# Performance work log

Measured on AMD Instinct MI355X. Metric: run time of the kernel, lower is better.

## Reference

```python
import jax, jax.numpy as jnp
import numpy as np

NUM_SCALES = 7
WEIGHTS = [1.0] * 7


def get_m(r, c):
    # r, c: [B, H, W] float coords; density map is [B, a, a], a = min(H, W)
    B, H, W = r.shape
    a = min(H, W)
    N = H * W
    xf = jnp.clip(jnp.floor(r), 0, a - 1).astype(jnp.int32)
    yf = jnp.clip(jnp.floor(c), 0, a - 1).astype(jnp.int32)
    xc = jnp.clip(jnp.ceil(r), 0, a - 1).astype(jnp.int32)
    yc = jnp.clip(jnp.ceil(c), 0, a - 1).astype(jnp.int32)
    xw = r - xf.astype(r.dtype)
    yw = c - yf.astype(c.dtype)
    w_tl = (1 - xw) * (1 - yw)
    w_tr = xw * (1 - yw)
    w_bl = (1 - xw) * yw
    w_br = xw * yw
    idx = jnp.concatenate([
        (xf * a + yf).reshape(B, N), (xc * a + yf).reshape(B, N),
        (xf * a + yc).reshape(B, N), (xc * a + yc).reshape(B, N)], axis=1)
    w = jnp.concatenate([
        w_tl.reshape(B, N), w_tr.reshape(B, N),
        w_bl.reshape(B, N), w_br.reshape(B, N)], axis=1)
    dm = jnp.zeros((B, a * a), dtype=r.dtype)
    dm = dm.at[jnp.arange(B)[:, None], idx].add(w)
    return dm.reshape(B, a, a)


def masked_bce(pred, tgt):
    # torch F.binary_cross_entropy clamps log terms at -100
    p = pred.reshape(-1)
    t = tgt.reshape(-1)
    log_p = jnp.clip(jnp.log(p), -100.0, None)
    log_1mp = jnp.clip(jnp.log(1.0 - p), -100.0, None)
    bce = -(t * log_p + (1.0 - t) * log_1mp)
    valid = (t == 1.0).astype(p.dtype)
    return jnp.sum(bce * valid) / jnp.sum(valid)


def _multiscale_loss(r3, c3, r4, c4, target):
    B = target.shape[0]
    Ht, Wt = target.shape[2], target.shape[3]
    total = 0.0
    for i in range(NUM_SCALES):
        cm = get_m(r3[i], c3[i]) + get_m(r4[i], c4[i])
        cm = cm / cm.max()
        resized = jax.image.resize(cm[:, None, :, :], (B, 1, Ht, Wt), method='linear')
        total = total + WEIGHTS[i] * masked_bce(resized, target)
    return total


def setup_inputs() -> dict:
    key = jax.random.key(0)
    k1, k2, k3, k4, k5 = jax.random.split(key, 5)
    a = 512
    shp = (NUM_SCALES, 8, a, a)
    scale = float(a - 1)
    r3 = jax.random.uniform(k1, shp, dtype=jnp.float32) * scale
    c3 = jax.random.uniform(k2, shp, dtype=jnp.float32) * scale
    r4 = jax.random.uniform(k3, shp, dtype=jnp.float32) * scale
    c4 = jax.random.uniform(k4, shp, dtype=jnp.float32) * scale
    target = (jax.random.uniform(k5, (8, 1, a, a)) < 0.5).astype(jnp.float32)
    return {"r3": r3, "c3": c3, "r4": r4, "c4": c4, "target": target}


def reference(r3, c3, r4, c4, target):
    return _multiscale_loss(r3, c3, r4, c4, target)
```

## Files before the change

kernel.cpp:

```cpp
#include <hip/hip_runtime.h>
#include <math.h>

#define A      512
#define NB     8
#define NS     7
#define AA     (A*A)
#define PPS    (NB*AA)
#define RPS    15
#define NSTRIP 35
#define LROWS  16
#define NIMG   (NS*NB)
#define NBKT   (NIMG*NSTRIP)
#define CAP    16896
#define BIN_THR 256
#define PTS_PER_BLOCK 4096
#define SPLAT_THR 512
#define SCALE_F   33554432.0f
#define INV_SCALE (1.0f/33554432.0f)
#define MAXB   1024
#define BCEB   2048

#define PARTS_OFF_F  2048
#define PARTS2_OFF_F 12288
#define NVAL_OFF_F   12800
#define BCEP_OFF_F   16384
#define DM_OFF_F     32768
#define BKT_OFF    ((size_t)DM_OFF_F * 4 + (size_t)NS * PPS * 4)
#define PER_IMG_B  ((size_t)NSTRIP * CAP * 8)

__global__ void init_kernel(float* __restrict__ ws) {
    if (blockIdx.x == 0) {
        for (int i = threadIdx.x; i < 2048; i += 128) ws[i] = 0.f;
        return;
    }
    int bkt = blockIdx.x - 1;
    int img = bkt / NSTRIP, k = bkt % NSTRIP;
    float4* row = (float4*)(ws + DM_OFF_F + (size_t)img * AA + (k * RPS) * A);
    row[threadIdx.x] = make_float4(0, 0, 0, 0);
}

__global__ void __launch_bounds__(BIN_THR)
bin_kernel(const float4* __restrict__ r3, const float4* __restrict__ c3,
           const float4* __restrict__ r4, const float4* __restrict__ c4,
           unsigned* __restrict__ cursors, float2* __restrict__ buckets,
           int img0) {
    const int limg = blockIdx.y;
    const int img  = img0 + limg;
    const float4* rp = blockIdx.z ? r4 : r3;
    const float4* cp = blockIdx.z ? c4 : c3;
    const int qbase = img * (AA / 4) + blockIdx.x * (PTS_PER_BLOCK / 4);

    float4 r[4], c[4];
#pragma unroll
    for (int j = 0; j < 4; j++) {
        int q = qbase + j * BIN_THR + threadIdx.x;
        r[j] = rp[q]; c[j] = cp[q];
    }

    __shared__ unsigned lcur[NSTRIP], lbase[NSTRIP];
    if (threadIdx.x < NSTRIP) lcur[threadIdx.x] = 0;
    __syncthreads();

    unsigned slot[16];
#define ALLOC(idx, rv) slot[idx] = atomicAdd(&lcur[(int)(rv) / RPS], 1u)
#pragma unroll
    for (int j = 0; j < 4; j++) {
        ALLOC(j * 4 + 0, r[j].x); ALLOC(j * 4 + 1, r[j].y);
        ALLOC(j * 4 + 2, r[j].z); ALLOC(j * 4 + 3, r[j].w);
    }
#undef ALLOC
    __syncthreads();

    if (threadIdx.x < NSTRIP)
        lbase[threadIdx.x] =
            atomicAdd(&cursors[img * NSTRIP + threadIdx.x], lcur[threadIdx.x]);
    __syncthreads();

    const int lbkt0 = limg * NSTRIP;
#define EMIT(idx, rv, cv) {                                                   \
        int s = (int)(rv) / RPS;                                              \
        unsigned sl = lbase[s] + slot[idx];                                   \
        if (sl < CAP)                                                         \
            buckets[(size_t)(lbkt0 + s) * CAP + sl] = make_float2(rv, cv); }
#pragma unroll
    for (int j = 0; j < 4; j++) {
        EMIT(j * 4 + 0, r[j].x, c[j].x); EMIT(j * 4 + 1, r[j].y, c[j].y);
        EMIT(j * 4 + 2, r[j].z, c[j].z); EMIT(j * 4 + 3, r[j].w, c[j].w);
    }
#undef EMIT
}

__device__ __forceinline__ void splat_pt(unsigned long long cp[2][LROWS][A/2],
                                         int g0, float r, float c) {
    int xf = (int)r, yf = (int)c;
    float xw = r - (float)xf, yw = c - (float)yf;
    float omx = 1.f - xw, omy = 1.f - yw;
    unsigned q0 = (unsigned)(omx * omy * SCALE_F + 0.5f);
    unsigned q1 = (unsigned)(omx * yw  * SCALE_F + 0.5f);
    unsigned q2 = (unsigned)(xw  * omy * SCALE_F + 0.5f);
    unsigned q3 = (unsigned)(xw  * yw  * SCALE_F + 0.5f);
    int lr = xf - g0, sel = yf & 1, pp = yf >> 1;
    atomicAdd(&cp[sel][lr    ][pp], ((unsigned long long)q1 << 32) | q0);
    atomicAdd(&cp[sel][lr + 1][pp], ((unsigned long long)q3 << 32) | q2);
}

__device__ __forceinline__ void combine4(unsigned long long cp[2][LROWS][A/2],
                                         int j, int c4, float v[4]) {
#pragma unroll
    for (int t = 0; t < 4; t++) {
        int cc = c4 + t;
        unsigned long long e = cp[0][j][cc >> 1];
        unsigned s = (cc & 1) ? (unsigned)(e >> 32) : (unsigned)e;
        if (cc & 1) s += (unsigned)cp[1][j][cc >> 1];
        else if (cc >= 2) s += (unsigned)(cp[1][j][(cc >> 1) - 1] >> 32);
        v[t] = (float)s * INV_SCALE;
    }
}

__global__ void __launch_bounds__(SPLAT_THR)
splat_dense(const float2* __restrict__ buckets, const unsigned* __restrict__ cursors,
            float* __restrict__ dm, const float4* __restrict__ tgt,
            float4* __restrict__ parts, int img0) {
    __shared__ unsigned long long cp[2][LROWS][A / 2];
    __shared__ float sr[8][3];
    const int lbkt = blockIdx.x;
    const int limg = lbkt / NSTRIP, k = lbkt % NSTRIP;
    const int img  = img0 + limg;
    const int b    = img & 7;
    const int g0   = k * RPS;

    unsigned long long* z = &cp[0][0][0];
    for (int i = threadIdx.x; i < 2 * LROWS * (A / 2); i += SPLAT_THR) z[i] = 0ull;
    __syncthreads();

    unsigned n = cursors[img * NSTRIP + k]; if (n > CAP) n = CAP;
    const float4* bp4 = (const float4*)(buckets + (size_t)lbkt * CAP);
    unsigned n2 = (n + 1) >> 1;
    for (unsigned i = threadIdx.x; i < n2; i += SPLAT_THR) {
        float4 q = bp4[i];
        splat_pt(cp, g0, q.x, q.y);
        if (2 * i + 1 < n) splat_pt(cp, g0, q.z, q.w);
    }
    __syncthreads();

    float* dimg = dm + (size_t)img * AA;
    for (int u = threadIdx.x; u < 2 * (A / 4); u += SPLAT_THR) {
        int j = (u >= (A / 4)) ? RPS : 0;
        int c4 = (u & (A / 4 - 1)) << 2;
        int gr = g0 + j;
        if (gr >= A) continue;
        float v[4];
        combine4(cp, j, c4, v);
        float* dst = dimg + gr * A + c4;
        unsafeAtomicAdd(dst + 0, v[0]); unsafeAtomicAdd(dst + 1, v[1]);
        unsafeAtomicAdd(dst + 2, v[2]); unsafeAtomicAdd(dst + 3, v[3]);
    }

    float S = 0.f, Np = 0.f, mxv = 0.f;
    const float4* timg = tgt + (size_t)b * (AA / 4);
    for (int u = threadIdx.x; u < (RPS - 1) * (A / 4); u += SPLAT_THR) {
        int j = 1 + (u >> 7), cq = u & 127, gr = g0 + j;
        if (gr >= A) continue;
        float v[4];
        combine4(cp, j, cq << 2, v);
        mxv = fmaxf(mxv, fmaxf(fmaxf(v[0], v[1]), fmaxf(v[2], v[3])));
        float4 t = timg[gr * (A / 4) + cq];
        if (t.x == 1.f && v[0] > 0.f) { S += __logf(v[0]); Np += 1.f; }
        if (t.y == 1.f && v[1] > 0.f) { S += __logf(v[1]); Np += 1.f; }
        if (t.z == 1.f && v[2] > 0.f) { S += __logf(v[2]); Np += 1.f; }
        if (t.w == 1.f && v[3] > 0.f) { S += __logf(v[3]); Np += 1.f; }
    }
    for (int off = 32; off > 0; off >>= 1) {
        S += __shfl_down(S, off); Np += __shfl_down(Np, off);
        mxv = fmaxf(mxv, __shfl_down(mxv, off));
    }
    int lane = threadIdx.x & 63, w = threadIdx.x >> 6;
    if (lane == 0) { sr[w][0] = S; sr[w][1] = Np; sr[w][2] = mxv; }
    __syncthreads();
    if (threadIdx.x == 0) {
        for (int ww = 1; ww < 8; ww++) {
            S += sr[ww][0]; Np += sr[ww][1]; mxv = fmaxf(mxv, sr[ww][2]);
        }
        parts[img * NSTRIP + k] = make_float4(S, Np, mxv, 0.f);
    }
}

__global__ void __launch_bounds__(256)
cleanup_kernel(const float* __restrict__ dm, const float4* __restrict__ tgt,
               float4* __restrict__ parts2, float* __restrict__ nval) {
    const int bx = blockIdx.x;
    float a0 = 0.f, a1 = 0.f, a2 = 0.f;
    if (bx < NIMG) {
        const int img = bx, b = img & 7;
        const float4* dimg = (const float4*)(dm + (size_t)img * AA);
        const float4* timg = tgt + (size_t)b * (AA / 4);
        for (int u = threadIdx.x; u < NSTRIP * (A / 4); u += 256) {
            int kk = u >> 7, cq = u & 127, gr = kk * RPS;
            float4 d = dimg[gr * (A / 4) + cq];
            float4 t = timg[gr * (A / 4) + cq];
            a2 = fmaxf(a2, fmaxf(fmaxf(d.x, d.y), fmaxf(d.z, d.w)));
            if (t.x == 1.f && d.x > 0.f) { a0 += __logf(d.x); a1 += 1.f; }
            if (t.y == 1.f && d.y > 0.f) { a0 += __logf(d.y); a1 += 1.f; }
            if (t.z == 1.f && d.z > 0.f) { a0 += __logf(d.z); a1 += 1.f; }
            if (t.w == 1.f && d.w > 0.f) { a0 += __logf(d.w); a1 += 1.f; }
        }
    } else {
        const float4* timg = tgt + (size_t)(bx - NIMG) * (AA / 4);
        for (int u = threadIdx.x; u < AA / 4; u += 256) {
            float4 t = timg[u];
            a0 += ((t.x == 1.f) ? 1.f : 0.f) + ((t.y == 1.f) ? 1.f : 0.f) +
                  ((t.z == 1.f) ? 1.f : 0.f) + ((t.w == 1.f) ? 1.f : 0.f);
        }
    }
    for (int off = 32; off > 0; off >>= 1) {
        a0 += __shfl_down(a0, off); a1 += __shfl_down(a1, off);
        a2 = fmaxf(a2, __shfl_down(a2, off));
    }
    __shared__ float sr[4][3];
    int lane = threadIdx.x & 63, w = threadIdx.x >> 6;
    if (lane == 0) { sr[w][0] = a0; sr[w][1] = a1; sr[w][2] = a2; }
    __syncthreads();
    if (threadIdx.x == 0) {
        for (int ww = 1; ww < 4; ww++) {
            a0 += sr[ww][0]; a1 += sr[ww][1]; a2 = fmaxf(a2, sr[ww][2]);
        }
        if (bx < NIMG) parts2[bx] = make_float4(a0, a1, a2, 0.f);
        else           nval[bx - NIMG] = a0;
    }
}

__global__ void __launch_bounds__(256)
final_fused(const float4* __restrict__ parts, const float4* __restrict__ parts2,
            const float* __restrict__ nval, float* __restrict__ out) {
    __shared__ float red[4][3];
    __shared__ float ps[NS][3];
    const int lane = threadIdx.x & 63, w = threadIdx.x >> 6;
    for (int s = 0; s < NS; s++) {
        float S = 0.f, Np = 0.f, Mx = 0.f;
        for (int t = threadIdx.x; t < NB * NSTRIP; t += 256) {
            float4 p = parts[s * NB * NSTRIP + t];
            S += p.x; Np += p.y; Mx = fmaxf(Mx, p.z);
        }
        if (threadIdx.x < NB) {
            float4 p = parts2[s * NB + threadIdx.x];
            S += p.x; Np += p.y; Mx = fmaxf(Mx, p.z);
        }
        for (int off = 32; off > 0; off >>= 1) {
            S += __shfl_down(S, off); Np += __shfl_down(Np, off);
            Mx = fmaxf(Mx, __shfl_down(Mx, off));
        }
        if (lane == 0) { red[w][0] = S; red[w][1] = Np; red[w][2] = Mx; }
        __syncthreads();
        if (threadIdx.x == 0) {
            for (int ww = 1; ww < 4; ww++) {
                S += red[ww][0]; Np += red[ww][1]; Mx = fmaxf(Mx, red[ww][2]);
            }
            ps[s][0] = S; ps[s][1] = Np; ps[s][2] = Mx;
        }
        __syncthreads();
    }
    if (threadIdx.x == 0) {
        float Nv = 0.f;
        for (int b = 0; b < NB; b++) Nv += nval[b];
        float t = 0.f;
        for (int s = 0; s < NS; s++) {
            float lm = __logf(ps[s][2]);
            t += (ps[s][1] * lm - ps[s][0] + 100.f * (Nv - ps[s][1])) / Nv;
        }
        out[0] = t;
    }
}

__device__ __forceinline__ void splat_lds_f(float lds[LROWS][A], int g0, unsigned k,
                                            float r, float c) {
    int xf = (int)r;
    if ((unsigned)xf / RPS != k) return;
    int yf = (int)c;
    float xw = r - (float)xf, yw = c - (float)yf;
    float omx = 1.f - xw, omy = 1.f - yw;
    int lr = xf - g0;
    atomicAdd(&lds[lr    ][yf    ], omx * omy);
    atomicAdd(&lds[lr + 1][yf    ], xw  * omy);
    atomicAdd(&lds[lr    ][yf + 1], omx * yw);
    atomicAdd(&lds[lr + 1][yf + 1], xw  * yw);
}

__global__ void __launch_bounds__(SPLAT_THR)
splat_gather(const float4* __restrict__ r3, const float4* __restrict__ c3,
             const float4* __restrict__ r4, const float4* __restrict__ c4,
             float* __restrict__ dm) {
    __shared__ float lds[LROWS][A];
    const unsigned k = blockIdx.x;
    const int img = blockIdx.y, tid = threadIdx.x, g0 = (int)k * RPS;
    float4* l4 = (float4*)&lds[0][0];
    for (int i = tid; i < LROWS * A / 4; i += SPLAT_THR) l4[i] = make_float4(0, 0, 0, 0);
    __syncthreads();
    const int qbase = img * (AA / 4);
    for (int i = tid; i < AA / 4; i += SPLAT_THR) {
        float4 ra = r3[qbase + i], ca = c3[qbase + i];
        float4 rb = r4[qbase + i], cb = c4[qbase + i];
        splat_lds_f(lds, g0, k, ra.x, ca.x); splat_lds_f(lds, g0, k, ra.y, ca.y);
        splat_lds_f(lds, g0, k, ra.z, ca.z); splat_lds_f(lds, g0, k, ra.w, ca.w);
        splat_lds_f(lds, g0, k, rb.x, cb.x); splat_lds_f(lds, g0, k, rb.y, cb.y);
        splat_lds_f(lds, g0, k, rb.z, cb.z); splat_lds_f(lds, g0, k, rb.w, cb.w);
    }
    __syncthreads();
    float* dimg = dm + (size_t)img * AA;
    for (int u = tid; u < LROWS * (A / 4); u += SPLAT_THR) {
        int j = u >> 7, cq = u & 127, gr = g0 + j;
        if (gr >= A) continue;
        float4 v = ((float4*)&lds[j][0])[cq];
        float* dst = dimg + gr * A + cq * 4;
        if (j == 0 || j == RPS) {
            unsafeAtomicAdd(dst + 0, v.x); unsafeAtomicAdd(dst + 1, v.y);
            unsafeAtomicAdd(dst + 2, v.z); unsafeAtomicAdd(dst + 3, v.w);
        } else {
            *(float4*)dst = v;
        }
    }
}

__global__ void max_kernel(const float4* __restrict__ dm, float* __restrict__ maxp) {
    int s = blockIdx.y;
    const float4* p = dm + (size_t)s * (PPS / 4);
    float m = 0.f;
    for (int i = blockIdx.x * blockDim.x + threadIdx.x; i < PPS / 4;
         i += gridDim.x * blockDim.x) {
        float4 v = p[i];
        m = fmaxf(m, fmaxf(fmaxf(v.x, v.y), fmaxf(v.z, v.w)));
    }
    for (int off = 32; off > 0; off >>= 1) m = fmaxf(m, __shfl_down(m, off));
    __shared__ float sm[4];
    if ((threadIdx.x & 63) == 0) sm[threadIdx.x >> 6] = m;
    __syncthreads();
    if (threadIdx.x == 0)
        maxp[s * MAXB + blockIdx.x] = fmaxf(fmaxf(sm[0], sm[1]), fmaxf(sm[2], sm[3]));
}

__global__ void max2_kernel(const float* __restrict__ maxp, float* __restrict__ mx) {
    int s = blockIdx.x;
    float m = 0.f;
    for (int i = threadIdx.x; i < MAXB; i += 256) m = fmaxf(m, maxp[s * MAXB + i]);
    for (int off = 32; off > 0; off >>= 1) m = fmaxf(m, __shfl_down(m, off));
    __shared__ float sm[4];
    if ((threadIdx.x & 63) == 0) sm[threadIdx.x >> 6] = m;
    __syncthreads();
    if (threadIdx.x == 0)
        mx[s] = fmaxf(fmaxf(sm[0], sm[1]), fmaxf(sm[2], sm[3]));
}

__global__ void __launch_bounds__(256)
bce_kernel(const float4* __restrict__ dm, const float4* __restrict__ tgt,
           const float* __restrict__ mx, float* __restrict__ bcep) {
    float lm[NS];
#pragma unroll
    for (int s = 0; s < NS; s++) lm[s] = __logf(mx[s]);
    float acc[NS];
#pragma unroll
    for (int s = 0; s < NS; s++) acc[s] = 0.f;
    float count = 0.f;
    const int NQ = PPS / 4;
    for (int i = blockIdx.x * blockDim.x + threadIdx.x; i < NQ;
         i += gridDim.x * blockDim.x) {
        float4 t = tgt[i];
        float vx = (t.x == 1.f) ? 1.f : 0.f;
        float vy = (t.y == 1.f) ? 1.f : 0.f;
        float vz = (t.z == 1.f) ? 1.f : 0.f;
        float vw = (t.w == 1.f) ? 1.f : 0.f;
        count += vx + vy + vz + vw;
#pragma unroll
        for (int s = 0; s < NS; s++) {
            float4 d = dm[s * NQ + i];
            acc[s] -= fmaxf(__logf(d.x) - lm[s], -100.f) * vx;
            acc[s] -= fmaxf(__logf(d.y) - lm[s], -100.f) * vy;
            acc[s] -= fmaxf(__logf(d.z) - lm[s], -100.f) * vz;
            acc[s] -= fmaxf(__logf(d.w) - lm[s], -100.f) * vw;
        }
    }
    for (int off = 32; off > 0; off >>= 1) {
#pragma unroll
        for (int s = 0; s < NS; s++) acc[s] += __shfl_down(acc[s], off);
        count += __shfl_down(count, off);
    }
    __shared__ float sred[4][NS + 1];
    int lane = threadIdx.x & 63, w = threadIdx.x >> 6;
    if (lane == 0) {
#pragma unroll
        for (int s = 0; s < NS; s++) sred[w][s] = acc[s];
        sred[w][NS] = count;
    }
    __syncthreads();
    if (threadIdx.x == 0) {
        for (int ww = 1; ww < 4; ww++) {
#pragma unroll
            for (int s = 0; s < NS; s++) acc[s] += sred[ww][s];
            count += sred[ww][NS];
        }
#pragma unroll
        for (int s = 0; s < NS; s++) bcep[blockIdx.x * 8 + s] = acc[s];
        bcep[blockIdx.x * 8 + NS] = count;
    }
}

__global__ void final_kernel(const float* __restrict__ bcep, float* __restrict__ out) {
    float acc[8];
#pragma unroll
    for (int c = 0; c < 8; c++) acc[c] = 0.f;
    for (int row = threadIdx.x; row < BCEB; row += 256) {
#pragma unroll
        for (int c = 0; c < 8; c++) acc[c] += bcep[row * 8 + c];
    }
    for (int off = 32; off > 0; off >>= 1) {
#pragma unroll
        for (int c = 0; c < 8; c++) acc[c] += __shfl_down(acc[c], off);
    }
    __shared__ float sred[4][8];
    int lane = threadIdx.x & 63, w = threadIdx.x >> 6;
    if (lane == 0) {
#pragma unroll
        for (int c = 0; c < 8; c++) sred[w][c] = acc[c];
    }
    __syncthreads();
    if (threadIdx.x == 0) {
        for (int ww = 1; ww < 4; ww++)
#pragma unroll
            for (int c = 0; c < 8; c++) acc[c] += sred[ww][c];
        float t = 0.f;
        for (int s = 0; s < NS; s++) t += acc[s] / acc[NS];
        out[0] = t;
    }
}

extern "C" void kernel_launch(void* const* d_in, const int* in_sizes, int n_in,
                              void* d_out, int out_size, void* d_ws, size_t ws_size,
                              hipStream_t stream) {
    const float* r3  = (const float*)d_in[0];
    const float* c3  = (const float*)d_in[1];
    const float* r4  = (const float*)d_in[2];
    const float* c4  = (const float*)d_in[3];
    const float* tgt = (const float*)d_in[4];
    float* out = (float*)d_out;

    float* ws         = (float*)d_ws;
    float* mx         = ws;
    unsigned* cursors = (unsigned*)d_ws + 16;
    float4* parts     = (float4*)(ws + PARTS_OFF_F);
    float4* parts2    = (float4*)(ws + PARTS2_OFF_F);
    float* nval       = ws + NVAL_OFF_F;
    float* maxp       = ws + PARTS_OFF_F;
    float* bcep       = ws + BCEP_OFF_F;
    float* dm         = ws + DM_OFF_F;

    size_t avail = (ws_size > BKT_OFF) ? ws_size - BKT_OFF : 0;
    int P = (int)(avail / PER_IMG_B);
    if (P > NIMG) P = NIMG;

    if (P >= 6) {
        float2* buckets = (float2*)((char*)d_ws + BKT_OFF);
        init_kernel<<<NBKT + 1, 128, 0, stream>>>(ws);
        for (int img0 = 0; img0 < NIMG; img0 += P) {
            int pc = NIMG - img0; if (pc > P) pc = P;
            bin_kernel<<<dim3(AA / PTS_PER_BLOCK, pc, 2), BIN_THR, 0, stream>>>(
                (const float4*)r3, (const float4*)c3,
                (const float4*)r4, (const float4*)c4, cursors, buckets, img0);
            splat_dense<<<pc * NSTRIP, SPLAT_THR, 0, stream>>>(
                buckets, cursors, dm, (const float4*)tgt, parts, img0);
        }
        cleanup_kernel<<<NIMG + NB, 256, 0, stream>>>(
            dm, (const float4*)tgt, parts2, nval);
        final_fused<<<1, 256, 0, stream>>>(parts, parts2, nval, out);
    } else {
        hipMemsetAsync(d_ws, 0, 8192, stream);
        hipMemsetAsync(dm, 0, (size_t)NS * PPS * sizeof(float), stream);
        splat_gather<<<dim3(NSTRIP, NIMG), SPLAT_THR, 0, stream>>>(
            (const float4*)r3, (const float4*)c3,
            (const float4*)r4, (const float4*)c4, dm);
        max_kernel<<<dim3(MAXB, NS), 256, 0, stream>>>((const float4*)dm, maxp);
        max2_kernel<<<NS, 256, 0, stream>>>(maxp, mx);
        bce_kernel<<<BCEB, 256, 0, stream>>>((const float4*)dm, (const float4*)tgt,
                                             mx, bcep);
        final_kernel<<<1, 256, 0, stream>>>(bcep, out);
    }
}
```

Baseline: 417.1 us.

## Duplicate strip-boundary points into neighbor buckets to drop global density-map atomics

```diff
diff --git a/kernel.cpp b/kernel.cpp
--- a/kernel.cpp
+++ b/kernel.cpp
@@ -6,12 +6,12 @@
 #define NS     7
 #define AA     (A*A)
 #define PPS    (NB*AA)
-#define RPS    15
-#define NSTRIP 35
-#define LROWS  16
+#define RPS    13
+#define NSTRIP 40
+#define LROWS  15
 #define NIMG   (NS*NB)
 #define NBKT   (NIMG*NSTRIP)
-#define CAP    16896
+#define CAP    15872
 #define BIN_THR 256
 #define PTS_PER_BLOCK 4096
 #define SPLAT_THR 512
@@ -20,23 +20,32 @@
 #define MAXB   1024
 #define BCEB   2048
 
-#define PARTS_OFF_F  2048
-#define PARTS2_OFF_F 12288
-#define NVAL_OFF_F   12800
-#define BCEP_OFF_F   16384
+#define NVALP_OFF_F  4096
+#define PARTS_OFF_F  8192
 #define DM_OFF_F     32768
-#define BKT_OFF    ((size_t)DM_OFF_F * 4 + (size_t)NS * PPS * 4)
-#define PER_IMG_B  ((size_t)NSTRIP * CAP * 8)
-
-__global__ void init_kernel(float* __restrict__ ws) {
+#define BKT_OFF      131072
+#define PER_IMG_B    ((size_t)NSTRIP * CAP * 8)
+
+__global__ void __launch_bounds__(256)
+init_kernel(unsigned* __restrict__ cursors, const float4* __restrict__ tgt,
+            float* __restrict__ nvalp) {
     if (blockIdx.x == 0) {
-        for (int i = threadIdx.x; i < 2048; i += 128) ws[i] = 0.f;
+        for (int i = threadIdx.x; i < NBKT; i += 256) cursors[i] = 0u;
         return;
     }
-    int bkt = blockIdx.x - 1;
-    int img = bkt / NSTRIP, k = bkt % NSTRIP;
-    float4* row = (float4*)(ws + DM_OFF_F + (size_t)img * AA + (k * RPS) * A);
-    row[threadIdx.x] = make_float4(0, 0, 0, 0);
+    const int base = (blockIdx.x - 1) * ((NB * AA / 4) / 64);
+    float a = 0.f;
+    for (int t = threadIdx.x; t < (NB * AA / 4) / 64; t += 256) {
+        float4 v = tgt[base + t];
+        a += ((v.x == 1.f) ? 1.f : 0.f) + ((v.y == 1.f) ? 1.f : 0.f) +
+             ((v.z == 1.f) ? 1.f : 0.f) + ((v.w == 1.f) ? 1.f : 0.f);
+    }
+    for (int off = 32; off > 0; off >>= 1) a += __shfl_down(a, off);
+    __shared__ float sm[4];
+    if ((threadIdx.x & 63) == 0) sm[threadIdx.x >> 6] = a;
+    __syncthreads();
+    if (threadIdx.x == 0)
+        nvalp[blockIdx.x - 1] = sm[0] + sm[1] + sm[2] + sm[3];
 }
 
 __global__ void __launch_bounds__(BIN_THR)
@@ -61,8 +70,12 @@
     if (threadIdx.x < NSTRIP) lcur[threadIdx.x] = 0;
     __syncthreads();
 
-    unsigned slot[16];
-#define ALLOC(idx, rv) slot[idx] = atomicAdd(&lcur[(int)(rv) / RPS], 1u)
+    unsigned slot[16], slot2[16];
+#define ALLOC(idx, rv) {                                                      \
+        int xf = (int)(rv); int s0 = xf / RPS;                                \
+        slot[idx] = atomicAdd(&lcur[s0], 1u);                                 \
+        slot2[idx] = (xf - s0 * RPS == RPS - 1)                               \
+                         ? atomicAdd(&lcur[s0 + 1], 1u) : 0u; }
 #pragma unroll
     for (int j = 0; j < 4; j++) {
         ALLOC(j * 4 + 0, r[j].x); ALLOC(j * 4 + 1, r[j].y);
@@ -78,10 +91,15 @@
 
     const int lbkt0 = limg * NSTRIP;
 #define EMIT(idx, rv, cv) {                                                   \
-        int s = (int)(rv) / RPS;                                              \
-        unsigned sl = lbase[s] + slot[idx];                                   \
+        int xf = (int)(rv); int s0 = xf / RPS;                                \
+        unsigned sl = lbase[s0] + slot[idx];                                  \
         if (sl < CAP)                                                         \
-            buckets[(size_t)(lbkt0 + s) * CAP + sl] = make_float2(rv, cv); }
+            buckets[(size_t)(lbkt0 + s0) * CAP + sl] = make_float2(rv, cv);   \
+        if (xf - s0 * RPS == RPS - 1) {                                       \
+            unsigned s2 = lbase[s0 + 1] + slot2[idx];                         \
+            if (s2 < CAP)                                                     \
+                buckets[(size_t)(lbkt0 + s0 + 1) * CAP + s2] =                \
+                    make_float2(rv, cv); } }
 #pragma unroll
     for (int j = 0; j < 4; j++) {
         EMIT(j * 4 + 0, r[j].x, c[j].x); EMIT(j * 4 + 1, r[j].y, c[j].y);
@@ -91,7 +109,7 @@
 }
 
 __device__ __forceinline__ void splat_pt(unsigned long long cp[2][LROWS][A/2],
-                                         int g0, float r, float c) {
+                                         int g0m1, float r, float c) {
     int xf = (int)r, yf = (int)c;
     float xw = r - (float)xf, yw = c - (float)yf;
     float omx = 1.f - xw, omy = 1.f - yw;
@@ -99,7 +117,7 @@
     unsigned q1 = (unsigned)(omx * yw  * SCALE_F + 0.5f);
     unsigned q2 = (unsigned)(xw  * omy * SCALE_F + 0.5f);
     unsigned q3 = (unsigned)(xw  * yw  * SCALE_F + 0.5f);
-    int lr = xf - g0, sel = yf & 1, pp = yf >> 1;
+    int lr = xf - g0m1, sel = yf & 1, pp = yf >> 1;
     atomicAdd(&cp[sel][lr    ][pp], ((unsigned long long)q1 << 32) | q0);
     atomicAdd(&cp[sel][lr + 1][pp], ((unsigned long long)q3 << 32) | q2);
 }
@@ -119,15 +137,14 @@
 
 __global__ void __launch_bounds__(SPLAT_THR)
 splat_dense(const float2* __restrict__ buckets, const unsigned* __restrict__ cursors,
-            float* __restrict__ dm, const float4* __restrict__ tgt,
-            float4* __restrict__ parts, int img0) {
+            const float4* __restrict__ tgt, float4* __restrict__ parts, int img0) {
     __shared__ unsigned long long cp[2][LROWS][A / 2];
     __shared__ float sr[8][3];
     const int lbkt = blockIdx.x;
     const int limg = lbkt / NSTRIP, k = lbkt % NSTRIP;
     const int img  = img0 + limg;
     const int b    = img & 7;
-    const int g0   = k * RPS;
+    const int g0m1 = k * RPS - 1;
 
     unsigned long long* z = &cp[0][0][0];
     for (int i = threadIdx.x; i < 2 * LROWS * (A / 2); i += SPLAT_THR) z[i] = 0ull;
@@ -138,29 +155,16 @@
     unsigned n2 = (n + 1) >> 1;
     for (unsigned i = threadIdx.x; i < n2; i += SPLAT_THR) {
         float4 q = bp4[i];
-        splat_pt(cp, g0, q.x, q.y);
-        if (2 * i + 1 < n) splat_pt(cp, g0, q.z, q.w);
-    }
-    __syncthreads();
-
-    float* dimg = dm + (size_t)img * AA;
-    for (int u = threadIdx.x; u < 2 * (A / 4); u += SPLAT_THR) {
-        int j = (u >= (A / 4)) ? RPS : 0;
-        int c4 = (u & (A / 4 - 1)) << 2;
-        int gr = g0 + j;
-        if (gr >= A) continue;
-        float v[4];
-        combine4(cp, j, c4, v);
-        float* dst = dimg + gr * A + c4;
-        unsafeAtomicAdd(dst + 0, v[0]); unsafeAtomicAdd(dst + 1, v[1]);
-        unsafeAtomicAdd(dst + 2, v[2]); unsafeAtomicAdd(dst + 3, v[3]);
-    }
-
+        splat_pt(cp, g0m1, q.x, q.y);
+        if (2 * i + 1 < n) splat_pt(cp, g0m1, q.z, q.w);
+    }
+    __syncthreads();
+
+    const int rows_owned = (A - k * RPS < RPS) ? (A - k * RPS) : RPS;
     float S = 0.f, Np = 0.f, mxv = 0.f;
     const float4* timg = tgt + (size_t)b * (AA / 4);
-    for (int u = threadIdx.x; u < (RPS - 1) * (A / 4); u += SPLAT_THR) {
-        int j = 1 + (u >> 7), cq = u & 127, gr = g0 + j;
-        if (gr >= A) continue;
+    for (int u = threadIdx.x; u < rows_owned * (A / 4); u += SPLAT_THR) {
+        int j = 1 + (u >> 7), cq = u & 127, gr = k * RPS + (u >> 7);
         float v[4];
         combine4(cp, j, cq << 2, v);
         mxv = fmaxf(mxv, fmaxf(fmaxf(v[0], v[1]), fmaxf(v[2], v[3])));
@@ -186,52 +190,8 @@
 }
 
 __global__ void __launch_bounds__(256)
-cleanup_kernel(const float* __restrict__ dm, const float4* __restrict__ tgt,
-               float4* __restrict__ parts2, float* __restrict__ nval) {
-    const int bx = blockIdx.x;
-    float a0 = 0.f, a1 = 0.f, a2 = 0.f;
-    if (bx < NIMG) {
-        const int img = bx, b = img & 7;
-        const float4* dimg = (const float4*)(dm + (size_t)img * AA);
-        const float4* timg = tgt + (size_t)b * (AA / 4);
-        for (int u = threadIdx.x; u < NSTRIP * (A / 4); u += 256) {
-            int kk = u >> 7, cq = u & 127, gr = kk * RPS;
-            float4 d = dimg[gr * (A / 4) + cq];
-            float4 t = timg[gr * (A / 4) + cq];
-            a2 = fmaxf(a2, fmaxf(fmaxf(d.x, d.y), fmaxf(d.z, d.w)));
-            if (t.x == 1.f && d.x > 0.f) { a0 += __logf(d.x); a1 += 1.f; }
-            if (t.y == 1.f && d.y > 0.f) { a0 += __logf(d.y); a1 += 1.f; }
-            if (t.z == 1.f && d.z > 0.f) { a0 += __logf(d.z); a1 += 1.f; }
-            if (t.w == 1.f && d.w > 0.f) { a0 += __logf(d.w); a1 += 1.f; }
-        }
-    } else {
-        const float4* timg = tgt + (size_t)(bx - NIMG) * (AA / 4);
-        for (int u = threadIdx.x; u < AA / 4; u += 256) {
-            float4 t = timg[u];
-            a0 += ((t.x == 1.f) ? 1.f : 0.f) + ((t.y == 1.f) ? 1.f : 0.f) +
-                  ((t.z == 1.f) ? 1.f : 0.f) + ((t.w == 1.f) ? 1.f : 0.f);
-        }
-    }
-    for (int off = 32; off > 0; off >>= 1) {
-        a0 += __shfl_down(a0, off); a1 += __shfl_down(a1, off);
-        a2 = fmaxf(a2, __shfl_down(a2, off));
-    }
-    __shared__ float sr[4][3];
-    int lane = threadIdx.x & 63, w = threadIdx.x >> 6;
-    if (lane == 0) { sr[w][0] = a0; sr[w][1] = a1; sr[w][2] = a2; }
-    __syncthreads();
-    if (threadIdx.x == 0) {
-        for (int ww = 1; ww < 4; ww++) {
-            a0 += sr[ww][0]; a1 += sr[ww][1]; a2 = fmaxf(a2, sr[ww][2]);
-        }
-        if (bx < NIMG) parts2[bx] = make_float4(a0, a1, a2, 0.f);
-        else           nval[bx - NIMG] = a0;
-    }
-}
-
-__global__ void __launch_bounds__(256)
-final_fused(const float4* __restrict__ parts, const float4* __restrict__ parts2,
-            const float* __restrict__ nval, float* __restrict__ out) {
+final_fused(const float4* __restrict__ parts, const float* __restrict__ nvalp,
+            float* __restrict__ out) {
     __shared__ float red[4][3];
     __shared__ float ps[NS][3];
     const int lane = threadIdx.x & 63, w = threadIdx.x >> 6;
@@ -241,10 +201,6 @@
             float4 p = parts[s * NB * NSTRIP + t];
             S += p.x; Np += p.y; Mx = fmaxf(Mx, p.z);
         }
-        if (threadIdx.x < NB) {
-            float4 p = parts2[s * NB + threadIdx.x];
-            S += p.x; Np += p.y; Mx = fmaxf(Mx, p.z);
-        }
         for (int off = 32; off > 0; off >>= 1) {
             S += __shfl_down(S, off); Np += __shfl_down(Np, off);
             Mx = fmaxf(Mx, __shfl_down(Mx, off));
@@ -261,7 +217,7 @@
     }
     if (threadIdx.x == 0) {
         float Nv = 0.f;
-        for (int b = 0; b < NB; b++) Nv += nval[b];
+        for (int i = 0; i < 64; i++) Nv += nvalp[i];
         float t = 0.f;
         for (int s = 0; s < NS; s++) {
             float lm = __logf(ps[s][2]);
@@ -271,8 +227,8 @@
     }
 }
 
-__device__ __forceinline__ void splat_lds_f(float lds[LROWS][A], int g0, unsigned k,
-                                            float r, float c) {
+__device__ __forceinline__ void splat_lds_f(float lds[RPS + 1][A], int g0,
+                                            unsigned k, float r, float c) {
     int xf = (int)r;
     if ((unsigned)xf / RPS != k) return;
     int yf = (int)c;
@@ -289,11 +245,12 @@
 splat_gather(const float4* __restrict__ r3, const float4* __restrict__ c3,
              const float4* __restrict__ r4, const float4* __restrict__ c4,
              float* __restrict__ dm) {
-    __shared__ float lds[LROWS][A];
+    __shared__ float lds[RPS + 1][A];
     const unsigned k = blockIdx.x;
     const int img = blockIdx.y, tid = threadIdx.x, g0 = (int)k * RPS;
     float4* l4 = (float4*)&lds[0][0];
-    for (int i = tid; i < LROWS * A / 4; i += SPLAT_THR) l4[i] = make_float4(0, 0, 0, 0);
+    for (int i = tid; i < (RPS + 1) * A / 4; i += SPLAT_THR)
+        l4[i] = make_float4(0, 0, 0, 0);
     __syncthreads();
     const int qbase = img * (AA / 4);
     for (int i = tid; i < AA / 4; i += SPLAT_THR) {
@@ -306,7 +263,7 @@
     }
     __syncthreads();
     float* dimg = dm + (size_t)img * AA;
-    for (int u = tid; u < LROWS * (A / 4); u += SPLAT_THR) {
+    for (int u = tid; u < (RPS + 1) * (A / 4); u += SPLAT_THR) {
         int j = u >> 7, cq = u & 127, gr = g0 + j;
         if (gr >= A) continue;
         float4 v = ((float4*)&lds[j][0])[cq];
@@ -442,13 +399,12 @@
     float* out = (float*)d_out;
 
     float* ws         = (float*)d_ws;
+    unsigned* cursors = (unsigned*)d_ws + 16;
+    float* nvalp      = ws + NVALP_OFF_F;
+    float4* parts     = (float4*)(ws + PARTS_OFF_F);
     float* mx         = ws;
-    unsigned* cursors = (unsigned*)d_ws + 16;
-    float4* parts     = (float4*)(ws + PARTS_OFF_F);
-    float4* parts2    = (float4*)(ws + PARTS2_OFF_F);
-    float* nval       = ws + NVAL_OFF_F;
-    float* maxp       = ws + PARTS_OFF_F;
-    float* bcep       = ws + BCEP_OFF_F;
+    float* maxp       = ws + 2048;
+    float* bcep       = ws + 16384;
     float* dm         = ws + DM_OFF_F;
 
     size_t avail = (ws_size > BKT_OFF) ? ws_size - BKT_OFF : 0;
@@ -457,18 +413,16 @@
 
     if (P >= 6) {
         float2* buckets = (float2*)((char*)d_ws + BKT_OFF);
-        init_kernel<<<NBKT + 1, 128, 0, stream>>>(ws);
+        init_kernel<<<65, 256, 0, stream>>>(cursors, (const float4*)tgt, nvalp);
         for (int img0 = 0; img0 < NIMG; img0 += P) {
             int pc = NIMG - img0; if (pc > P) pc = P;
             bin_kernel<<<dim3(AA / PTS_PER_BLOCK, pc, 2), BIN_THR, 0, stream>>>(
                 (const float4*)r3, (const float4*)c3,
                 (const float4*)r4, (const float4*)c4, cursors, buckets, img0);
             splat_dense<<<pc * NSTRIP, SPLAT_THR, 0, stream>>>(
-                buckets, cursors, dm, (const float4*)tgt, parts, img0);
-        }
-        cleanup_kernel<<<NIMG + NB, 256, 0, stream>>>(
-            dm, (const float4*)tgt, parts2, nval);
-        final_fused<<<1, 256, 0, stream>>>(parts, parts2, nval, out);
+                buckets, cursors, (const float4*)tgt, parts, img0);
+        }
+        final_fused<<<1, 256, 0, stream>>>(parts, nvalp, out);
     } else {
         hipMemsetAsync(d_ws, 0, 8192, stream);
         hipMemsetAsync(dm, 0, (size_t)NS * PPS * sizeof(float), stream);
```

New measurement: 425.4 us. No clear change (+2.0%).
